# Optimization experiments

Hardware: AMD Instinct MI355X
Metric: run time of the kernel (lower is better)

The kernel has to match this reference:

```python
import jax, jax.numpy as jnp
import numpy as np

B, CIN, H, W = 32, 128, 64, 64
OUT, KH, KW = 256, 3, 3
NSK, SDIM = 4, 128


def setup_inputs() -> dict:
    key = jax.random.key(0)
    kx, kw_, kb, ks = jax.random.split(key, 4)
    x = jax.random.normal(kx, (B, CIN, H, W), dtype=jnp.float32)
    kval = float(np.sqrt(1.0 / (CIN * KH * KW)))  # groups=1
    weight = jax.random.uniform(kw_, (OUT, CIN, KH, KW), jnp.float32, -kval, kval)
    bias_tensor = jax.random.uniform(kb, (OUT,), jnp.float32, -kval, kval)
    # Rademacher / sketch_dim, shape (n, s, O) == torch's type1_signed_matrices
    signed = (2.0 * jax.random.bernoulli(ks, 0.5, (NSK, SDIM, OUT)).astype(jnp.float32) - 1.0) / SDIM
    # prod = einsum('ijkl,mi->mjkl') per sketch -> (n, s, Cin, kh, kw)
    prod = jnp.einsum('oikl,nso->nsikl', weight, signed)
    # .permute(2,3,1,0).flatten(0,2): (s,Cin,kh,kw) -> (kh,kw,Cin,s) -> (kh*kw*Cin, s)
    type1_sketches = prod.transpose(0, 3, 4, 2, 1).reshape(NSK, KH * KW * CIN, SDIM)
    return {
        "x": x,
        "type1_sketches": type1_sketches,
        "type1_signed_matrices": signed,
        "bias_tensor": bias_tensor,
    }


def reference(x, type1_sketches, type1_signed_matrices, bias_tensor):
    b, _, h1, w1 = x.shape
    h2 = h1 - KH + 1
    w2 = w1 - KW + 1
    # torch unfold: (B, Cin*KH*KW, E), features ordered channel-major (C, kh, kw)
    patches = jax.lax.conv_general_dilated_patches(
        x, filter_shape=(KH, KW), window_strides=(1, 1), padding='VALID'
    )  # (B, Cin*KH*KW, H2, W2)
    patches = patches.reshape(b, CIN * KH * KW, h2 * w2)  # (B, F, E)
    # 'bnfe,nfs->bnse' with the n-expansion folded away
    y = jnp.einsum('bfe,nfs->bnse', patches, type1_sketches)
    z = jnp.einsum('bnse,nso->bnoe', y, type1_signed_matrices)
    z = z.reshape(b, NSK, OUT, h2, w2)
    out = jnp.mean(z, axis=1) + bias_tensor[None, :, None, None]
    return out
```

## Files before the change

kernel.cpp:

```cpp
#include <hip/hip_runtime.h>
#include <hip/hip_bf16.h>
#include <stdint.h>


#define BATCH 32
#define CIN   128
#define HH    64
#define WW    64
#define OUTC  256
#define H2    62
#define W2    62
#define A_TILE 32768
#define WS_A_BYTES (18 * A_TILE)
#define BKHB  17408

typedef __bf16 bf16x8 __attribute__((ext_vector_type(8)));
typedef float  f32x4  __attribute__((ext_vector_type(4)));

typedef unsigned int u32_as1 __attribute__((address_space(1)));
typedef unsigned int u32_as3 __attribute__((address_space(3)));

__device__ __forceinline__ void async_copy16(const void* g, void* l) {
  __builtin_amdgcn_global_load_lds((const u32_as1*)g, (u32_as3*)l, 16, 0, 0);
}

#define FPB 4
__global__ __launch_bounds__(256) void weff_kernel(
    const float* __restrict__ sketches,
    const float* __restrict__ sgn,
    char* __restrict__ wsA)
{
  __shared__ alignas(16) float sk[512 * FPB];
  const int f0 = blockIdx.x * FPB;
  const int t  = threadIdx.x;

  for (int k = 0; k < (512 * FPB) / 256; ++k) {
    int idx = t + k * 256;
    int fi  = idx >> 9;
    int ns  = idx & 511;
    int n   = ns >> 7;
    int s   = ns & 127;
    sk[ns * FPB + fi] = sketches[(n * 1152 + f0 + fi) * 128 + s];
  }
  __syncthreads();

  const int o = t;
  float acc0 = 0.f, acc1 = 0.f, acc2 = 0.f, acc3 = 0.f;
#pragma unroll 8
  for (int ns = 0; ns < 512; ++ns) {
    float sg = sgn[ns * 256 + o];
    f32x4 skv = *(const f32x4*)(&sk[ns * FPB]);
    acc0 += sg * skv[0];
    acc1 += sg * skv[1];
    acc2 += sg * skv[2];
    acc3 += sg * skv[3];
  }

  float accs[FPB] = {acc0, acc1, acc2, acc3};
#pragma unroll
  for (int fi = 0; fi < FPB; ++fi) {
    int f    = f0 + fi;
    int c    = f / 9;
    int khkw = f - c * 9;
    int s    = khkw * 2 + (c >> 6);
    int kk   = c & 63;
    uint32_t byteoff = (uint32_t)s * A_TILE + (uint32_t)o * 128
                     + (((uint32_t)kk * 2u) ^ (uint32_t)((o & 7) << 4));
    *(__hip_bfloat16*)(wsA + byteoff) = __float2bfloat16(accs[fi] * 0.25f);
  }
}

__global__ __launch_bounds__(512, 2) void conv_kernel(
    const float* __restrict__ x,
    const char*  __restrict__ wA,
    const float* __restrict__ bias,
    float* __restrict__ out)
{
  __shared__ alignas(16) char lds[65536 + 4 * BKHB];
  char* ldsA = lds;
  char* ldsB = lds + 65536;

  const int bid = blockIdx.x;
  const int swz = (bid & 7) * 124 + (bid >> 3);
  const int b   = swz / 31;
  const int ip  = swz - b * 31;
  const int i0  = ip * 2;

  const int t    = threadIdx.x;
  const int lane = t & 63;
  const int w    = t >> 6;
  const int wo   = w >> 1;
  const int ir   = w & 1;

#define STAGE_A(LIN, BUF) do {                                             \
    const char* asrc_ = wA + (size_t)(LIN) * A_TILE + w * 1024 + lane * 16;\
    char* adst_ = ldsA + (BUF) * 32768 + w * 1024;                         \
    async_copy16(asrc_,          adst_);                                   \
    async_copy16(asrc_ + 8192,   adst_ + 8192);                            \
    async_copy16(asrc_ + 16384,  adst_ + 16384);                           \
    async_copy16(asrc_ + 24576,  adst_ + 24576);                           \
  } while (0)

  STAGE_A(0, 0);

  {
    const int j  = t & 63;
    const int cq = t >> 6;
    const uint32_t swb = (uint32_t)((j & 7) << 4);
#pragma unroll
    for (int r = 0; r < 4; ++r) {
      const float* xr = x + (((size_t)(b * CIN + cq * 16)) * HH + (i0 + r)) * WW + j;
      char* lrow = ldsB + r * BKHB + j * 256;
#pragma unroll
      for (int g = 0; g < 2; ++g) {
        bf16x8 pk;
#pragma unroll
        for (int cc = 0; cc < 8; ++cc)
          pk[cc] = (__bf16)xr[(size_t)(g * 8 + cc) * (HH * WW)];
        uint32_t c0b = (uint32_t)(cq * 32 + g * 16);
        *(bf16x8*)(lrow + (c0b ^ swb)) = pk;
      }
    }
    if (t < 256) {
      int r  = t >> 6;
      int pj = 64 + ((t >> 4) & 3);
      int sl = (t & 15) * 16;
      bf16x8 z = {};
      *(bf16x8*)(ldsB + r * BKHB + pj * 256 + sl) = z;
    }
  }

  f32x4 acc[4][4];
  const f32x4 zf = {0.f, 0.f, 0.f, 0.f};
#pragma unroll
  for (int mi = 0; mi < 4; ++mi)
#pragma unroll
    for (int ni = 0; ni < 4; ++ni)
      acc[mi][ni] = zf;

  __syncthreads();

  const int ln15  = lane & 15;
  const int khi16 = (lane >> 4) << 4;
  const uint32_t swa = (uint32_t)((ln15 & 7) << 4);
  const char* pAr = ldsA + (wo * 64 + ln15) * 128;
  const char* pA0 = pAr + (((uint32_t)khi16) ^ swa);
  const char* pA1 = pAr + (((uint32_t)(64 | khi16)) ^ swa);

#define MKB(KW, KS) (ldsB + ir * BKHB + (ln15 + (KW)) * 256                \
    + (((uint32_t)(((KS) << 6) | khi16)) ^ ((uint32_t)(((ln15 + (KW)) & 7) << 4))))
  const char* pB00 = MKB(0, 0); const char* pB01 = MKB(0, 1);
  const char* pB10 = MKB(1, 0); const char* pB11 = MKB(1, 1);
  const char* pB20 = MKB(2, 0); const char* pB21 = MKB(2, 1);
#undef MKB

#define MFMA_ __builtin_amdgcn_mfma_f32_16x16x32_bf16

#define KSBLK(LIN, KH, KW, KS) do {                                        \
    const int ai_ = ((LIN) & 1) * 32768;                                   \
    bf16x8 a0_ = *(const bf16x8*)(pA##KS + ai_);                           \
    bf16x8 a1_ = *(const bf16x8*)(pA##KS + ai_ + 2048);                    \
    bf16x8 a2_ = *(const bf16x8*)(pA##KS + ai_ + 4096);                    \
    bf16x8 a3_ = *(const bf16x8*)(pA##KS + ai_ + 6144);                    \
    const int bi_ = (KH) * BKHB + ((LIN) & 1) * 128;                       \
    bf16x8 b0_ = *(const bf16x8*)(pB##KW##KS + bi_);                       \
    bf16x8 b1_ = *(const bf16x8*)(pB##KW##KS + bi_ + 4096);                \
    bf16x8 b2_ = *(const bf16x8*)(pB##KW##KS + bi_ + 8192);                \
    bf16x8 b3_ = *(const bf16x8*)(pB##KW##KS + bi_ + 12288);               \
    acc[0][0] = MFMA_(a0_, b0_, acc[0][0], 0, 0, 0);                       \
    acc[0][1] = MFMA_(a0_, b1_, acc[0][1], 0, 0, 0);                       \
    acc[0][2] = MFMA_(a0_, b2_, acc[0][2], 0, 0, 0);                       \
    acc[0][3] = MFMA_(a0_, b3_, acc[0][3], 0, 0, 0);                       \
    acc[1][0] = MFMA_(a1_, b0_, acc[1][0], 0, 0, 0);                       \
    acc[1][1] = MFMA_(a1_, b1_, acc[1][1], 0, 0, 0);                       \
    acc[1][2] = MFMA_(a1_, b2_, acc[1][2], 0, 0, 0);                       \
    acc[1][3] = MFMA_(a1_, b3_, acc[1][3], 0, 0, 0);                       \
    acc[2][0] = MFMA_(a2_, b0_, acc[2][0], 0, 0, 0);                       \
    acc[2][1] = MFMA_(a2_, b1_, acc[2][1], 0, 0, 0);                       \
    acc[2][2] = MFMA_(a2_, b2_, acc[2][2], 0, 0, 0);                       \
    acc[2][3] = MFMA_(a2_, b3_, acc[2][3], 0, 0, 0);                       \
    acc[3][0] = MFMA_(a3_, b0_, acc[3][0], 0, 0, 0);                       \
    acc[3][1] = MFMA_(a3_, b1_, acc[3][1], 0, 0, 0);                       \
    acc[3][2] = MFMA_(a3_, b2_, acc[3][2], 0, 0, 0);                       \
    acc[3][3] = MFMA_(a3_, b3_, acc[3][3], 0, 0, 0);                       \
  } while (0)

#define STEP(LIN, KH, KW) do {                                             \
    if ((LIN) < 17) STAGE_A((LIN) + 1, ((LIN) + 1) & 1);                   \
    KSBLK(LIN, KH, KW, 0);                                                 \
    KSBLK(LIN, KH, KW, 1);                                                 \
    __syncthreads();                                                       \
  } while (0)

  STEP(0, 0, 0);   STEP(1, 0, 0);
  STEP(2, 0, 1);   STEP(3, 0, 1);
  STEP(4, 0, 2);   STEP(5, 0, 2);
  STEP(6, 1, 0);   STEP(7, 1, 0);
  STEP(8, 1, 1);   STEP(9, 1, 1);
  STEP(10, 1, 2);  STEP(11, 1, 2);
  STEP(12, 2, 0);  STEP(13, 2, 0);
  STEP(14, 2, 1);  STEP(15, 2, 1);
  STEP(16, 2, 2);  STEP(17, 2, 2);

#undef STEP
#undef KSBLK
#undef MFMA_
#undef STAGE_A

  const int jn   = ln15;
  const int g4   = lane >> 4;
  const int irow = i0 + ir;
#pragma unroll
  for (int mi = 0; mi < 4; ++mi) {
#pragma unroll
    for (int ni = 0; ni < 4; ++ni) {
      const int jj = (ni << 4) + jn;
      if (jj < W2) {
#pragma unroll
        for (int rr = 0; rr < 4; ++rr) {
          const int o = (wo << 6) + (mi << 4) + (g4 << 2) + rr;
          out[(((size_t)b * OUTC + o) * H2 + irow) * W2 + jj] = acc[mi][ni][rr] + bias[o];
        }
      }
    }
  }
}

extern "C" void kernel_launch(void* const* d_in, const int* in_sizes, int n_in,
                              void* d_out, int out_size, void* d_ws, size_t ws_size,
                              hipStream_t stream) {
  const float* x        = (const float*)d_in[0];
  const float* sketches = (const float*)d_in[1];
  const float* sgn      = (const float*)d_in[2];
  const float* bias     = (const float*)d_in[3];
  float* out            = (float*)d_out;
  char* wsA             = (char*)d_ws;

  if (ws_size < (size_t)WS_A_BYTES) return;

  weff_kernel<<<1152 / FPB, 256, 0, stream>>>(sketches, sgn, wsA);
  conv_kernel<<<BATCH * (H2 / 2), 512, 0, stream>>>(x, wsA, bias, out);
}
```

Before: 115.4 us.

## Prefetch two A stages ahead with explicit waitcnt and split barriers

Moves the weight-tile async copies two stages ahead and replaces the per-step __syncthreads with explicit vmcnt/lgkmcnt waits and raw s_barrier. All LDS fragments for a step are loaded into registers first, then the buffer is released and the next copy issued so it overlaps the MFMA block, which runs at raised priority. The aim is to hide global-to-LDS latency and cut barrier stalls. It relies on hand-counted vmcnt values matching the outstanding async copies, and it raises register pressure from holding 16 fragments at once.

```diff
diff --git a/kernel.cpp b/kernel.cpp
--- a/kernel.cpp
+++ b/kernel.cpp
@@ -102,6 +102,7 @@
   } while (0)
 
   STAGE_A(0, 0);
+  STAGE_A(1, 1);
 
   {
     const int j  = t & 63;
@@ -138,8 +139,6 @@
     for (int ni = 0; ni < 4; ++ni)
       acc[mi][ni] = zf;
 
-  __syncthreads();
-
   const int ln15  = lane & 15;
   const int khi16 = (lane >> 4) << 4;
   const uint32_t swa = (uint32_t)((ln15 & 7) << 4);
@@ -154,56 +153,88 @@
   const char* pB20 = MKB(2, 0); const char* pB21 = MKB(2, 1);
 #undef MKB
 
+  asm volatile("s_waitcnt lgkmcnt(0)" ::: "memory");
+
 #define MFMA_ __builtin_amdgcn_mfma_f32_16x16x32_bf16
-
-#define KSBLK(LIN, KH, KW, KS) do {                                        \
-    const int ai_ = ((LIN) & 1) * 32768;                                   \
-    bf16x8 a0_ = *(const bf16x8*)(pA##KS + ai_);                           \
-    bf16x8 a1_ = *(const bf16x8*)(pA##KS + ai_ + 2048);                    \
-    bf16x8 a2_ = *(const bf16x8*)(pA##KS + ai_ + 4096);                    \
-    bf16x8 a3_ = *(const bf16x8*)(pA##KS + ai_ + 6144);                    \
-    const int bi_ = (KH) * BKHB + ((LIN) & 1) * 128;                       \
-    bf16x8 b0_ = *(const bf16x8*)(pB##KW##KS + bi_);                       \
-    bf16x8 b1_ = *(const bf16x8*)(pB##KW##KS + bi_ + 4096);                \
-    bf16x8 b2_ = *(const bf16x8*)(pB##KW##KS + bi_ + 8192);                \
-    bf16x8 b3_ = *(const bf16x8*)(pB##KW##KS + bi_ + 12288);               \
-    acc[0][0] = MFMA_(a0_, b0_, acc[0][0], 0, 0, 0);                       \
-    acc[0][1] = MFMA_(a0_, b1_, acc[0][1], 0, 0, 0);                       \
-    acc[0][2] = MFMA_(a0_, b2_, acc[0][2], 0, 0, 0);                       \
-    acc[0][3] = MFMA_(a0_, b3_, acc[0][3], 0, 0, 0);                       \
-    acc[1][0] = MFMA_(a1_, b0_, acc[1][0], 0, 0, 0);                       \
-    acc[1][1] = MFMA_(a1_, b1_, acc[1][1], 0, 0, 0);                       \
-    acc[1][2] = MFMA_(a1_, b2_, acc[1][2], 0, 0, 0);                       \
-    acc[1][3] = MFMA_(a1_, b3_, acc[1][3], 0, 0, 0);                       \
-    acc[2][0] = MFMA_(a2_, b0_, acc[2][0], 0, 0, 0);                       \
-    acc[2][1] = MFMA_(a2_, b1_, acc[2][1], 0, 0, 0);                       \
-    acc[2][2] = MFMA_(a2_, b2_, acc[2][2], 0, 0, 0);                       \
-    acc[2][3] = MFMA_(a2_, b3_, acc[2][3], 0, 0, 0);                       \
-    acc[3][0] = MFMA_(a3_, b0_, acc[3][0], 0, 0, 0);                       \
-    acc[3][1] = MFMA_(a3_, b1_, acc[3][1], 0, 0, 0);                       \
-    acc[3][2] = MFMA_(a3_, b2_, acc[3][2], 0, 0, 0);                       \
-    acc[3][3] = MFMA_(a3_, b3_, acc[3][3], 0, 0, 0);                       \
+#define WAITVM4 asm volatile("s_waitcnt vmcnt(4)" ::: "memory")
+#define WAITVM0 asm volatile("s_waitcnt vmcnt(0)" ::: "memory")
+#define WAITLG0 asm volatile("s_waitcnt lgkmcnt(0)" ::: "memory")
+
+#define STEP(LIN, KH, KW, WVM) do {                                        \
+    WVM;                                                                   \
+    __builtin_amdgcn_s_barrier();                                          \
+    const int ai_  = ((LIN) & 1) * 32768;                                  \
+    const int chb_ = ((LIN) & 1) * 128 + (KH) * BKHB;                      \
+    bf16x8 aA0 = *(const bf16x8*)(pA0 + ai_);                              \
+    bf16x8 aA1 = *(const bf16x8*)(pA0 + ai_ + 2048);                       \
+    bf16x8 aA2 = *(const bf16x8*)(pA0 + ai_ + 4096);                       \
+    bf16x8 aA3 = *(const bf16x8*)(pA0 + ai_ + 6144);                       \
+    bf16x8 aB0 = *(const bf16x8*)(pA1 + ai_);                              \
+    bf16x8 aB1 = *(const bf16x8*)(pA1 + ai_ + 2048);                       \
+    bf16x8 aB2 = *(const bf16x8*)(pA1 + ai_ + 4096);                       \
+    bf16x8 aB3 = *(const bf16x8*)(pA1 + ai_ + 6144);                       \
+    bf16x8 bA0 = *(const bf16x8*)(pB##KW##0 + chb_);                       \
+    bf16x8 bA1 = *(const bf16x8*)(pB##KW##0 + chb_ + 4096);                \
+    bf16x8 bA2 = *(const bf16x8*)(pB##KW##0 + chb_ + 8192);                \
+    bf16x8 bA3 = *(const bf16x8*)(pB##KW##0 + chb_ + 12288);               \
+    bf16x8 bB0 = *(const bf16x8*)(pB##KW##1 + chb_);                       \
+    bf16x8 bB1 = *(const bf16x8*)(pB##KW##1 + chb_ + 4096);                \
+    bf16x8 bB2 = *(const bf16x8*)(pB##KW##1 + chb_ + 8192);                \
+    bf16x8 bB3 = *(const bf16x8*)(pB##KW##1 + chb_ + 12288);               \
+    WAITLG0;                                                               \
+    __builtin_amdgcn_sched_barrier(0);                                     \
+    __builtin_amdgcn_s_barrier();                                          \
+    if ((LIN) < 16) STAGE_A((LIN) + 2, (LIN) & 1);                         \
+    __builtin_amdgcn_s_setprio(1);                                         \
+    acc[0][0] = MFMA_(aA0, bA0, acc[0][0], 0, 0, 0);                       \
+    acc[0][1] = MFMA_(aA0, bA1, acc[0][1], 0, 0, 0);                       \
+    acc[0][2] = MFMA_(aA0, bA2, acc[0][2], 0, 0, 0);                       \
+    acc[0][3] = MFMA_(aA0, bA3, acc[0][3], 0, 0, 0);                       \
+    acc[1][0] = MFMA_(aA1, bA0, acc[1][0], 0, 0, 0);                       \
+    acc[1][1] = MFMA_(aA1, bA1, acc[1][1], 0, 0, 0);                       \
+    acc[1][2] = MFMA_(aA1, bA2, acc[1][2], 0, 0, 0);                       \
+    acc[1][3] = MFMA_(aA1, bA3, acc[1][3], 0, 0, 0);                       \
+    acc[2][0] = MFMA_(aA2, bA0, acc[2][0], 0, 0, 0);                       \
+    acc[2][1] = MFMA_(aA2, bA1, acc[2][1], 0, 0, 0);                       \
+    acc[2][2] = MFMA_(aA2, bA2, acc[2][2], 0, 0, 0);                       \
+    acc[2][3] = MFMA_(aA2, bA3, acc[2][3], 0, 0, 0);                       \
+    acc[3][0] = MFMA_(aA3, bA0, acc[3][0], 0, 0, 0);                       \
+    acc[3][1] = MFMA_(aA3, bA1, acc[3][1], 0, 0, 0);                       \
+    acc[3][2] = MFMA_(aA3, bA2, acc[3][2], 0, 0, 0);                       \
+    acc[3][3] = MFMA_(aA3, bA3, acc[3][3], 0, 0, 0);                       \
+    acc[0][0] = MFMA_(aB0, bB0, acc[0][0], 0, 0, 0);                       \
+    acc[0][1] = MFMA_(aB0, bB1, acc[0][1], 0, 0, 0);                       \
+    acc[0][2] = MFMA_(aB0, bB2, acc[0][2], 0, 0, 0);                       \
+    acc[0][3] = MFMA_(aB0, bB3, acc[0][3], 0, 0, 0);                       \
+    acc[1][0] = MFMA_(aB1, bB0, acc[1][0], 0, 0, 0);                       \
+    acc[1][1] = MFMA_(aB1, bB1, acc[1][1], 0, 0, 0);                       \
+    acc[1][2] = MFMA_(aB1, bB2, acc[1][2], 0, 0, 0);                       \
+    acc[1][3] = MFMA_(aB1, bB3, acc[1][3], 0, 0, 0);                       \
+    acc[2][0] = MFMA_(aB2, bB0, acc[2][0], 0, 0, 0);                       \
+    acc[2][1] = MFMA_(aB2, bB1, acc[2][1], 0, 0, 0);                       \
+    acc[2][2] = MFMA_(aB2, bB2, acc[2][2], 0, 0, 0);                       \
+    acc[2][3] = MFMA_(aB2, bB3, acc[2][3], 0, 0, 0);                       \
+    acc[3][0] = MFMA_(aB3, bB0, acc[3][0], 0, 0, 0);                       \
+    acc[3][1] = MFMA_(aB3, bB1, acc[3][1], 0, 0, 0);                       \
+    acc[3][2] = MFMA_(aB3, bB2, acc[3][2], 0, 0, 0);                       \
+    acc[3][3] = MFMA_(aB3, bB3, acc[3][3], 0, 0, 0);                       \
+    __builtin_amdgcn_s_setprio(0);                                         \
   } while (0)
 
-#define STEP(LIN, KH, KW) do {                                             \
-    if ((LIN) < 17) STAGE_A((LIN) + 1, ((LIN) + 1) & 1);                   \
-    KSBLK(LIN, KH, KW, 0);                                                 \
-    KSBLK(LIN, KH, KW, 1);                                                 \
-    __syncthreads();                                                       \
-  } while (0)
-
-  STEP(0, 0, 0);   STEP(1, 0, 0);
-  STEP(2, 0, 1);   STEP(3, 0, 1);
-  STEP(4, 0, 2);   STEP(5, 0, 2);
-  STEP(6, 1, 0);   STEP(7, 1, 0);
-  STEP(8, 1, 1);   STEP(9, 1, 1);
-  STEP(10, 1, 2);  STEP(11, 1, 2);
-  STEP(12, 2, 0);  STEP(13, 2, 0);
-  STEP(14, 2, 1);  STEP(15, 2, 1);
-  STEP(16, 2, 2);  STEP(17, 2, 2);
+  STEP(0, 0, 0, WAITVM4);   STEP(1, 0, 0, WAITVM4);
+  STEP(2, 0, 1, WAITVM4);   STEP(3, 0, 1, WAITVM4);
+  STEP(4, 0, 2, WAITVM4);   STEP(5, 0, 2, WAITVM4);
+  STEP(6, 1, 0, WAITVM4);   STEP(7, 1, 0, WAITVM4);
+  STEP(8, 1, 1, WAITVM4);   STEP(9, 1, 1, WAITVM4);
+  STEP(10, 1, 2, WAITVM4);  STEP(11, 1, 2, WAITVM4);
+  STEP(12, 2, 0, WAITVM4);  STEP(13, 2, 0, WAITVM4);
+  STEP(14, 2, 1, WAITVM4);  STEP(15, 2, 1, WAITVM4);
+  STEP(16, 2, 2, WAITVM4);  STEP(17, 2, 2, WAITVM0);
 
 #undef STEP
-#undef KSBLK
+#undef WAITLG0
+#undef WAITVM0
+#undef WAITVM4
 #undef MFMA_
 #undef STAGE_A
 
```

Result: slower. 129.0 us (+11.8%).

## Enlarge conv tile to four output rows with 128-channel warp tiles

Applied to the files above, without the earlier changes.

Each block now computes four output rows (16 row groups per image, 512 blocks) instead of two. Each warp covers 128 output channels by one row, using an 8x4 accumulator tile, so every B fragment is reused across twice as many A fragments. This halves the number of times each weight tile is staged per output and removes the final barrier. The row halo is clamped and the last-column fragment uses clamped pointers instead of zero padding. In exchange the kernel needs more registers and LDS (6 input rows), and the last row group computes rows that are discarded.

```diff
diff --git a/kernel.cpp b/kernel.cpp
--- a/kernel.cpp
+++ b/kernel.cpp
@@ -12,7 +12,7 @@
 #define W2    62
 #define A_TILE 32768
 #define WS_A_BYTES (18 * A_TILE)
-#define BKHB  17408
+#define BROWB 16384
 
 typedef __bf16 bf16x8 __attribute__((ext_vector_type(8)));
 typedef float  f32x4  __attribute__((ext_vector_type(4)));
@@ -76,21 +76,21 @@
     const float* __restrict__ bias,
     float* __restrict__ out)
 {
-  __shared__ alignas(16) char lds[65536 + 4 * BKHB];
+  __shared__ alignas(16) char lds[65536 + 6 * BROWB];
   char* ldsA = lds;
   char* ldsB = lds + 65536;
 
   const int bid = blockIdx.x;
-  const int swz = (bid & 7) * 124 + (bid >> 3);
-  const int b   = swz / 31;
-  const int ip  = swz - b * 31;
-  const int i0  = ip * 2;
+  const int swz = (bid & 7) * 64 + (bid >> 3);
+  const int b   = swz >> 4;
+  const int ig  = swz & 15;
+  const int i0  = ig * 4;
 
   const int t    = threadIdx.x;
   const int lane = t & 63;
   const int w    = t >> 6;
-  const int wo   = w >> 1;
-  const int ir   = w & 1;
+  const int wo   = w >> 2;
+  const int we   = w & 3;
 
 #define STAGE_A(LIN, BUF) do {                                             \
     const char* asrc_ = wA + (size_t)(LIN) * A_TILE + w * 1024 + lane * 16;\
@@ -108,9 +108,10 @@
     const int cq = t >> 6;
     const uint32_t swb = (uint32_t)((j & 7) << 4);
 #pragma unroll
-    for (int r = 0; r < 4; ++r) {
-      const float* xr = x + (((size_t)(b * CIN + cq * 16)) * HH + (i0 + r)) * WW + j;
-      char* lrow = ldsB + r * BKHB + j * 256;
+    for (int r = 0; r < 6; ++r) {
+      int xrow = i0 + r; if (xrow > 63) xrow = 63;
+      const float* xr = x + (((size_t)(b * CIN + cq * 16)) * HH + xrow) * WW + j;
+      char* lrow = ldsB + r * BROWB + j * 256;
 #pragma unroll
       for (int g = 0; g < 2; ++g) {
         bf16x8 pk;
@@ -121,52 +122,53 @@
         *(bf16x8*)(lrow + (c0b ^ swb)) = pk;
       }
     }
-    if (t < 256) {
-      int r  = t >> 6;
-      int pj = 64 + ((t >> 4) & 3);
-      int sl = (t & 15) * 16;
-      bf16x8 z = {};
-      *(bf16x8*)(ldsB + r * BKHB + pj * 256 + sl) = z;
-    }
-  }
-
-  f32x4 acc[4][4];
+  }
+
+  f32x4 acc[8][4];
   const f32x4 zf = {0.f, 0.f, 0.f, 0.f};
 #pragma unroll
-  for (int mi = 0; mi < 4; ++mi)
+  for (int mi = 0; mi < 8; ++mi)
 #pragma unroll
     for (int ni = 0; ni < 4; ++ni)
       acc[mi][ni] = zf;
-
-  __syncthreads();
 
   const int ln15  = lane & 15;
   const int khi16 = (lane >> 4) << 4;
   const uint32_t swa = (uint32_t)((ln15 & 7) << 4);
-  const char* pAr = ldsA + (wo * 64 + ln15) * 128;
+  const char* pAr = ldsA + (wo * 128 + ln15) * 128;
   const char* pA0 = pAr + (((uint32_t)khi16) ^ swa);
   const char* pA1 = pAr + (((uint32_t)(64 | khi16)) ^ swa);
 
-#define MKB(KW, KS) (ldsB + ir * BKHB + (ln15 + (KW)) * 256                \
-    + (((uint32_t)(((KS) << 6) | khi16)) ^ ((uint32_t)(((ln15 + (KW)) & 7) << 4))))
-  const char* pB00 = MKB(0, 0); const char* pB01 = MKB(0, 1);
-  const char* pB10 = MKB(1, 0); const char* pB11 = MKB(1, 1);
-  const char* pB20 = MKB(2, 0); const char* pB21 = MKB(2, 1);
+#define MKB(COL, KS) (ldsB + (we * 64 + (COL)) * 256                       \
+    + (((uint32_t)(((KS) << 6) | khi16)) ^ ((uint32_t)(((COL) & 7) << 4))))
+  const char* pB00 = MKB(ln15 + 0, 0); const char* pB01 = MKB(ln15 + 0, 1);
+  const char* pB10 = MKB(ln15 + 1, 0); const char* pB11 = MKB(ln15 + 1, 1);
+  const char* pB20 = MKB(ln15 + 2, 0); const char* pB21 = MKB(ln15 + 2, 1);
+  const int c30 = (48 + ln15 + 0 > 63) ? 63 : 48 + ln15 + 0;
+  const int c31 = (48 + ln15 + 1 > 63) ? 63 : 48 + ln15 + 1;
+  const int c32 = (48 + ln15 + 2 > 63) ? 63 : 48 + ln15 + 2;
+  const char* pC00 = MKB(c30, 0); const char* pC01 = MKB(c30, 1);
+  const char* pC10 = MKB(c31, 0); const char* pC11 = MKB(c31, 1);
+  const char* pC20 = MKB(c32, 0); const char* pC21 = MKB(c32, 1);
 #undef MKB
 
+  __syncthreads();
+
 #define MFMA_ __builtin_amdgcn_mfma_f32_16x16x32_bf16
 
-#define KSBLK(LIN, KH, KW, KS) do {                                        \
-    const int ai_ = ((LIN) & 1) * 32768;                                   \
-    bf16x8 a0_ = *(const bf16x8*)(pA##KS + ai_);                           \
-    bf16x8 a1_ = *(const bf16x8*)(pA##KS + ai_ + 2048);                    \
-    bf16x8 a2_ = *(const bf16x8*)(pA##KS + ai_ + 4096);                    \
-    bf16x8 a3_ = *(const bf16x8*)(pA##KS + ai_ + 6144);                    \
-    const int bi_ = (KH) * BKHB + ((LIN) & 1) * 128;                       \
-    bf16x8 b0_ = *(const bf16x8*)(pB##KW##KS + bi_);                       \
-    bf16x8 b1_ = *(const bf16x8*)(pB##KW##KS + bi_ + 4096);                \
-    bf16x8 b2_ = *(const bf16x8*)(pB##KW##KS + bi_ + 8192);                \
-    bf16x8 b3_ = *(const bf16x8*)(pB##KW##KS + bi_ + 12288);               \
+#define KSH(AP, BP, CP, IMM, AIMM) do {                                    \
+    bf16x8 b0_ = *(const bf16x8*)((BP) + (IMM));                           \
+    bf16x8 b1_ = *(const bf16x8*)((BP) + (IMM) + 4096);                    \
+    bf16x8 b2_ = *(const bf16x8*)((BP) + (IMM) + 8192);                    \
+    bf16x8 b3_ = *(const bf16x8*)((CP) + (IMM));                           \
+    bf16x8 a0_ = *(const bf16x8*)((AP) + (AIMM));                          \
+    bf16x8 a1_ = *(const bf16x8*)((AP) + (AIMM) + 2048);                   \
+    bf16x8 a2_ = *(const bf16x8*)((AP) + (AIMM) + 4096);                   \
+    bf16x8 a3_ = *(const bf16x8*)((AP) + (AIMM) + 6144);                   \
+    bf16x8 a4_ = *(const bf16x8*)((AP) + (AIMM) + 8192);                   \
+    bf16x8 a5_ = *(const bf16x8*)((AP) + (AIMM) + 10240);                  \
+    bf16x8 a6_ = *(const bf16x8*)((AP) + (AIMM) + 12288);                  \
+    bf16x8 a7_ = *(const bf16x8*)((AP) + (AIMM) + 14336);                  \
     acc[0][0] = MFMA_(a0_, b0_, acc[0][0], 0, 0, 0);                       \
     acc[0][1] = MFMA_(a0_, b1_, acc[0][1], 0, 0, 0);                       \
     acc[0][2] = MFMA_(a0_, b2_, acc[0][2], 0, 0, 0);                       \
@@ -183,13 +185,31 @@
     acc[3][1] = MFMA_(a3_, b1_, acc[3][1], 0, 0, 0);                       \
     acc[3][2] = MFMA_(a3_, b2_, acc[3][2], 0, 0, 0);                       \
     acc[3][3] = MFMA_(a3_, b3_, acc[3][3], 0, 0, 0);                       \
+    acc[4][0] = MFMA_(a4_, b0_, acc[4][0], 0, 0, 0);                       \
+    acc[4][1] = MFMA_(a4_, b1_, acc[4][1], 0, 0, 0);                       \
+    acc[4][2] = MFMA_(a4_, b2_, acc[4][2], 0, 0, 0);                       \
+    acc[4][3] = MFMA_(a4_, b3_, acc[4][3], 0, 0, 0);                       \
+    acc[5][0] = MFMA_(a5_, b0_, acc[5][0], 0, 0, 0);                       \
+    acc[5][1] = MFMA_(a5_, b1_, acc[5][1], 0, 0, 0);                       \
+    acc[5][2] = MFMA_(a5_, b2_, acc[5][2], 0, 0, 0);                       \
+    acc[5][3] = MFMA_(a5_, b3_, acc[5][3], 0, 0, 0);                       \
+    acc[6][0] = MFMA_(a6_, b0_, acc[6][0], 0, 0, 0);                       \
+    acc[6][1] = MFMA_(a6_, b1_, acc[6][1], 0, 0, 0);                       \
+    acc[6][2] = MFMA_(a6_, b2_, acc[6][2], 0, 0, 0);                       \
+    acc[6][3] = MFMA_(a6_, b3_, acc[6][3], 0, 0, 0);                       \
+    acc[7][0] = MFMA_(a7_, b0_, acc[7][0], 0, 0, 0);                       \
+    acc[7][1] = MFMA_(a7_, b1_, acc[7][1], 0, 0, 0);                       \
+    acc[7][2] = MFMA_(a7_, b2_, acc[7][2], 0, 0, 0);                       \
+    acc[7][3] = MFMA_(a7_, b3_, acc[7][3], 0, 0, 0);                       \
   } while (0)
 
 #define STEP(LIN, KH, KW) do {                                             \
     if ((LIN) < 17) STAGE_A((LIN) + 1, ((LIN) + 1) & 1);                   \
-    KSBLK(LIN, KH, KW, 0);                                                 \
-    KSBLK(LIN, KH, KW, 1);                                                 \
-    __syncthreads();                                                       \
+    KSH(pA0, pB##KW##0, pC##KW##0,                                         \
+        (KH) * BROWB + ((LIN) & 1) * 128, ((LIN) & 1) * 32768);            \
+    KSH(pA1, pB##KW##1, pC##KW##1,                                         \
+        (KH) * BROWB + ((LIN) & 1) * 128, ((LIN) & 1) * 32768);            \
+    if ((LIN) < 17) __syncthreads();                                       \
   } while (0)
 
   STEP(0, 0, 0);   STEP(1, 0, 0);
@@ -203,23 +223,26 @@
   STEP(16, 2, 2);  STEP(17, 2, 2);
 
 #undef STEP
-#undef KSBLK
+#undef KSH
 #undef MFMA_
 #undef STAGE_A
 
   const int jn   = ln15;
   const int g4   = lane >> 4;
-  const int irow = i0 + ir;
-#pragma unroll
-  for (int mi = 0; mi < 4; ++mi) {
-#pragma unroll
-    for (int ni = 0; ni < 4; ++ni) {
-      const int jj = (ni << 4) + jn;
-      if (jj < W2) {
-#pragma unroll
-        for (int rr = 0; rr < 4; ++rr) {
-          const int o = (wo << 6) + (mi << 4) + (g4 << 2) + rr;
-          out[(((size_t)b * OUTC + o) * H2 + irow) * W2 + jj] = acc[mi][ni][rr] + bias[o];
+  const int irow = i0 + we;
+  if (irow < H2) {
+#pragma unroll
+    for (int mi = 0; mi < 8; ++mi) {
+#pragma unroll
+      for (int ni = 0; ni < 4; ++ni) {
+        const int jj = (ni << 4) + jn;
+        if (jj < W2) {
+#pragma unroll
+          for (int rr = 0; rr < 4; ++rr) {
+            const int o = (wo << 7) + (mi << 4) + (g4 << 2) + rr;
+            out[(((size_t)b * OUTC + o) * H2 + irow) * W2 + jj] =
+                acc[mi][ni][rr] + bias[o];
+          }
         }
       }
     }
@@ -239,5 +262,5 @@
   if (ws_size < (size_t)WS_A_BYTES) return;
 
   weff_kernel<<<1152 / FPB, 256, 0, stream>>>(sketches, sgn, wsA);
-  conv_kernel<<<BATCH * (H2 / 2), 512, 0, stream>>>(x, wsA, bias, out);
-}
+  conv_kernel<<<BATCH * 16, 512, 0, stream>>>(x, wsA, bias, out);
+}
```

Result: faster. 106.5 us (-7.7%).

## Retile conv kernel to one output row per block with finer weight stages

Applied to the files above, without the earlier changes.

The conv kernel now has each 256-thread block compute a single output row instead of two, with 4 waves each owning 64 output channels. The weight matrix is re-laid out in the workspace into 36 smaller stages (32 channels per stage) in a fragment-friendly order, so A operand loads are contiguous per lane without XOR swizzle. The last N-tile clamps column indices instead of zero-padding LDS, and MFMA bursts are wrapped in s_setprio. Input rows are no longer shared between two output rows, so each block stages three input rows for one output row, and the extra stages add more barriers.

```diff
diff --git a/kernel.cpp b/kernel.cpp
--- a/kernel.cpp
+++ b/kernel.cpp
@@ -10,9 +10,9 @@
 #define OUTC  256
 #define H2    62
 #define W2    62
-#define A_TILE 32768
-#define WS_A_BYTES (18 * A_TILE)
-#define BKHB  17408
+#define A_TILE 16384
+#define WS_A_BYTES (36 * A_TILE)
+#define BROWB 16384
 
 typedef __bf16 bf16x8 __attribute__((ext_vector_type(8)));
 typedef float  f32x4  __attribute__((ext_vector_type(4)));
@@ -59,46 +59,44 @@
   float accs[FPB] = {acc0, acc1, acc2, acc3};
 #pragma unroll
   for (int fi = 0; fi < FPB; ++fi) {
-    int f    = f0 + fi;
-    int c    = f / 9;
-    int khkw = f - c * 9;
-    int s    = khkw * 2 + (c >> 6);
-    int kk   = c & 63;
-    uint32_t byteoff = (uint32_t)s * A_TILE + (uint32_t)o * 128
-                     + (((uint32_t)kk * 2u) ^ (uint32_t)((o & 7) << 4));
+    int f   = f0 + fi;
+    int c   = f / 9;
+    int tap = f - c * 9;
+    int st  = tap * 4 + (c >> 5);
+    int kk  = c & 31;
+    uint32_t byteoff = (uint32_t)st * A_TILE + (uint32_t)(o >> 4) * 1024
+                     + (uint32_t)(((kk >> 3) * 16 + (o & 15)) * 16)
+                     + (uint32_t)((kk & 7) * 2);
     *(__hip_bfloat16*)(wsA + byteoff) = __float2bfloat16(accs[fi] * 0.25f);
   }
 }
 
-__global__ __launch_bounds__(512, 2) void conv_kernel(
+__global__ __launch_bounds__(256, 2) void conv_kernel(
     const float* __restrict__ x,
     const char*  __restrict__ wA,
     const float* __restrict__ bias,
     float* __restrict__ out)
 {
-  __shared__ alignas(16) char lds[65536 + 4 * BKHB];
+  __shared__ alignas(16) char lds[2 * A_TILE + 3 * BROWB];
   char* ldsA = lds;
-  char* ldsB = lds + 65536;
+  char* ldsB = lds + 2 * A_TILE;
 
   const int bid = blockIdx.x;
-  const int swz = (bid & 7) * 124 + (bid >> 3);
-  const int b   = swz / 31;
-  const int ip  = swz - b * 31;
-  const int i0  = ip * 2;
+  const int swz = (bid & 7) * 248 + (bid >> 3);
+  const int b   = swz / H2;
+  const int i   = swz - b * H2;
 
   const int t    = threadIdx.x;
   const int lane = t & 63;
   const int w    = t >> 6;
-  const int wo   = w >> 1;
-  const int ir   = w & 1;
-
-#define STAGE_A(LIN, BUF) do {                                             \
-    const char* asrc_ = wA + (size_t)(LIN) * A_TILE + w * 1024 + lane * 16;\
-    char* adst_ = ldsA + (BUF) * 32768 + w * 1024;                         \
-    async_copy16(asrc_,          adst_);                                   \
-    async_copy16(asrc_ + 8192,   adst_ + 8192);                            \
-    async_copy16(asrc_ + 16384,  adst_ + 16384);                           \
-    async_copy16(asrc_ + 24576,  adst_ + 24576);                           \
+
+#define STAGE_A(ST, BUF) do {                                              \
+    const char* asrc_ = wA + (size_t)(ST) * A_TILE + w * 4096 + lane * 16; \
+    char* adst_ = ldsA + (BUF) * A_TILE + w * 4096;                        \
+    async_copy16(asrc_,         adst_);                                    \
+    async_copy16(asrc_ + 1024,  adst_ + 1024);                             \
+    async_copy16(asrc_ + 2048,  adst_ + 2048);                             \
+    async_copy16(asrc_ + 3072,  adst_ + 3072);                             \
   } while (0)
 
   STAGE_A(0, 0);
@@ -108,26 +106,19 @@
     const int cq = t >> 6;
     const uint32_t swb = (uint32_t)((j & 7) << 4);
 #pragma unroll
-    for (int r = 0; r < 4; ++r) {
-      const float* xr = x + (((size_t)(b * CIN + cq * 16)) * HH + (i0 + r)) * WW + j;
-      char* lrow = ldsB + r * BKHB + j * 256;
-#pragma unroll
-      for (int g = 0; g < 2; ++g) {
+    for (int r = 0; r < 3; ++r) {
+      const float* xr = x + (((size_t)(b * CIN + cq * 32)) * HH + (i + r)) * WW + j;
+      char* lrow = ldsB + r * BROWB + j * 256;
+#pragma unroll
+      for (int g = 0; g < 4; ++g) {
         bf16x8 pk;
 #pragma unroll
         for (int cc = 0; cc < 8; ++cc)
           pk[cc] = (__bf16)xr[(size_t)(g * 8 + cc) * (HH * WW)];
-        uint32_t c0b = (uint32_t)(cq * 32 + g * 16);
+        uint32_t c0b = (uint32_t)(cq * 64 + g * 16);
         *(bf16x8*)(lrow + (c0b ^ swb)) = pk;
       }
     }
-    if (t < 256) {
-      int r  = t >> 6;
-      int pj = 64 + ((t >> 4) & 3);
-      int sl = (t & 15) * 16;
-      bf16x8 z = {};
-      *(bf16x8*)(ldsB + r * BKHB + pj * 256 + sl) = z;
-    }
   }
 
   f32x4 acc[4][4];
@@ -138,35 +129,40 @@
     for (int ni = 0; ni < 4; ++ni)
       acc[mi][ni] = zf;
 
-  __syncthreads();
-
   const int ln15  = lane & 15;
   const int khi16 = (lane >> 4) << 4;
-  const uint32_t swa = (uint32_t)((ln15 & 7) << 4);
-  const char* pAr = ldsA + (wo * 64 + ln15) * 128;
-  const char* pA0 = pAr + (((uint32_t)khi16) ^ swa);
-  const char* pA1 = pAr + (((uint32_t)(64 | khi16)) ^ swa);
-
-#define MKB(KW, KS) (ldsB + ir * BKHB + (ln15 + (KW)) * 256                \
-    + (((uint32_t)(((KS) << 6) | khi16)) ^ ((uint32_t)(((ln15 + (KW)) & 7) << 4))))
-  const char* pB00 = MKB(0, 0); const char* pB01 = MKB(0, 1);
-  const char* pB10 = MKB(1, 0); const char* pB11 = MKB(1, 1);
-  const char* pB20 = MKB(2, 0); const char* pB21 = MKB(2, 1);
+  const char* pA = ldsA + w * 4096 + lane * 16;
+
+#define MKB(COL, PAR) (ldsB + (COL) * 256                                  \
+    + (uint32_t)((((PAR) * 64) | khi16) ^ (((COL) & 7) << 4)))
+  const char* pB00 = MKB(ln15 + 0, 0); const char* pB01 = MKB(ln15 + 0, 1);
+  const char* pB10 = MKB(ln15 + 1, 0); const char* pB11 = MKB(ln15 + 1, 1);
+  const char* pB20 = MKB(ln15 + 2, 0); const char* pB21 = MKB(ln15 + 2, 1);
+  const int c30 = (48 + ln15 + 0 > 63) ? 63 : 48 + ln15 + 0;
+  const int c31 = (48 + ln15 + 1 > 63) ? 63 : 48 + ln15 + 1;
+  const int c32 = (48 + ln15 + 2 > 63) ? 63 : 48 + ln15 + 2;
+  const char* pC00 = MKB(c30, 0); const char* pC01 = MKB(c30, 1);
+  const char* pC10 = MKB(c31, 0); const char* pC11 = MKB(c31, 1);
+  const char* pC20 = MKB(c32, 0); const char* pC21 = MKB(c32, 1);
 #undef MKB
 
+  __syncthreads();
+
 #define MFMA_ __builtin_amdgcn_mfma_f32_16x16x32_bf16
 
-#define KSBLK(LIN, KH, KW, KS) do {                                        \
-    const int ai_ = ((LIN) & 1) * 32768;                                   \
-    bf16x8 a0_ = *(const bf16x8*)(pA##KS + ai_);                           \
-    bf16x8 a1_ = *(const bf16x8*)(pA##KS + ai_ + 2048);                    \
-    bf16x8 a2_ = *(const bf16x8*)(pA##KS + ai_ + 4096);                    \
-    bf16x8 a3_ = *(const bf16x8*)(pA##KS + ai_ + 6144);                    \
-    const int bi_ = (KH) * BKHB + ((LIN) & 1) * 128;                       \
-    bf16x8 b0_ = *(const bf16x8*)(pB##KW##KS + bi_);                       \
-    bf16x8 b1_ = *(const bf16x8*)(pB##KW##KS + bi_ + 4096);                \
-    bf16x8 b2_ = *(const bf16x8*)(pB##KW##KS + bi_ + 8192);                \
-    bf16x8 b3_ = *(const bf16x8*)(pB##KW##KS + bi_ + 12288);               \
+#define STEP(ST, KH, KW, CK2, PAR) do {                                    \
+    if ((ST) < 35) STAGE_A((ST) + 1, ((ST) + 1) & 1);                      \
+    const int ab_ = ((ST) & 1) * A_TILE;                                   \
+    const int bi_ = (KH) * BROWB + (CK2) * 128;                            \
+    bf16x8 b0_ = *(const bf16x8*)(pB##KW##PAR + bi_);                      \
+    bf16x8 b1_ = *(const bf16x8*)(pB##KW##PAR + bi_ + 4096);               \
+    bf16x8 b2_ = *(const bf16x8*)(pB##KW##PAR + bi_ + 8192);               \
+    bf16x8 b3_ = *(const bf16x8*)(pC##KW##PAR + bi_);                      \
+    bf16x8 a0_ = *(const bf16x8*)(pA + ab_);                               \
+    bf16x8 a1_ = *(const bf16x8*)(pA + ab_ + 1024);                        \
+    bf16x8 a2_ = *(const bf16x8*)(pA + ab_ + 2048);                        \
+    bf16x8 a3_ = *(const bf16x8*)(pA + ab_ + 3072);                        \
+    __builtin_amdgcn_s_setprio(1);                                         \
     acc[0][0] = MFMA_(a0_, b0_, acc[0][0], 0, 0, 0);                       \
     acc[0][1] = MFMA_(a0_, b1_, acc[0][1], 0, 0, 0);                       \
     acc[0][2] = MFMA_(a0_, b2_, acc[0][2], 0, 0, 0);                       \
@@ -183,33 +179,35 @@
     acc[3][1] = MFMA_(a3_, b1_, acc[3][1], 0, 0, 0);                       \
     acc[3][2] = MFMA_(a3_, b2_, acc[3][2], 0, 0, 0);                       \
     acc[3][3] = MFMA_(a3_, b3_, acc[3][3], 0, 0, 0);                       \
+    __builtin_amdgcn_s_setprio(0);                                         \
+    if ((ST) < 35) __syncthreads();                                        \
   } while (0)
 
-#define STEP(LIN, KH, KW) do {                                             \
-    if ((LIN) < 17) STAGE_A((LIN) + 1, ((LIN) + 1) & 1);                   \
-    KSBLK(LIN, KH, KW, 0);                                                 \
-    KSBLK(LIN, KH, KW, 1);                                                 \
-    __syncthreads();                                                       \
-  } while (0)
-
-  STEP(0, 0, 0);   STEP(1, 0, 0);
-  STEP(2, 0, 1);   STEP(3, 0, 1);
-  STEP(4, 0, 2);   STEP(5, 0, 2);
-  STEP(6, 1, 0);   STEP(7, 1, 0);
-  STEP(8, 1, 1);   STEP(9, 1, 1);
-  STEP(10, 1, 2);  STEP(11, 1, 2);
-  STEP(12, 2, 0);  STEP(13, 2, 0);
-  STEP(14, 2, 1);  STEP(15, 2, 1);
-  STEP(16, 2, 2);  STEP(17, 2, 2);
+  STEP(0,  0, 0, 0, 0);  STEP(1,  0, 0, 0, 1);
+  STEP(2,  0, 0, 1, 0);  STEP(3,  0, 0, 1, 1);
+  STEP(4,  0, 1, 0, 0);  STEP(5,  0, 1, 0, 1);
+  STEP(6,  0, 1, 1, 0);  STEP(7,  0, 1, 1, 1);
+  STEP(8,  0, 2, 0, 0);  STEP(9,  0, 2, 0, 1);
+  STEP(10, 0, 2, 1, 0);  STEP(11, 0, 2, 1, 1);
+  STEP(12, 1, 0, 0, 0);  STEP(13, 1, 0, 0, 1);
+  STEP(14, 1, 0, 1, 0);  STEP(15, 1, 0, 1, 1);
+  STEP(16, 1, 1, 0, 0);  STEP(17, 1, 1, 0, 1);
+  STEP(18, 1, 1, 1, 0);  STEP(19, 1, 1, 1, 1);
+  STEP(20, 1, 2, 0, 0);  STEP(21, 1, 2, 0, 1);
+  STEP(22, 1, 2, 1, 0);  STEP(23, 1, 2, 1, 1);
+  STEP(24, 2, 0, 0, 0);  STEP(25, 2, 0, 0, 1);
+  STEP(26, 2, 0, 1, 0);  STEP(27, 2, 0, 1, 1);
+  STEP(28, 2, 1, 0, 0);  STEP(29, 2, 1, 0, 1);
+  STEP(30, 2, 1, 1, 0);  STEP(31, 2, 1, 1, 1);
+  STEP(32, 2, 2, 0, 0);  STEP(33, 2, 2, 0, 1);
+  STEP(34, 2, 2, 1, 0);  STEP(35, 2, 2, 1, 1);
 
 #undef STEP
-#undef KSBLK
 #undef MFMA_
 #undef STAGE_A
 
-  const int jn   = ln15;
-  const int g4   = lane >> 4;
-  const int irow = i0 + ir;
+  const int jn = ln15;
+  const int g4 = lane >> 4;
 #pragma unroll
   for (int mi = 0; mi < 4; ++mi) {
 #pragma unroll
@@ -218,8 +216,9 @@
       if (jj < W2) {
 #pragma unroll
         for (int rr = 0; rr < 4; ++rr) {
-          const int o = (wo << 6) + (mi << 4) + (g4 << 2) + rr;
-          out[(((size_t)b * OUTC + o) * H2 + irow) * W2 + jj] = acc[mi][ni][rr] + bias[o];
+          const int o = (w << 6) + (mi << 4) + (g4 << 2) + rr;
+          out[(((size_t)b * OUTC + o) * H2 + i) * W2 + jj] =
+              acc[mi][ni][rr] + bias[o];
         }
       }
     }
@@ -239,5 +238,5 @@
   if (ws_size < (size_t)WS_A_BYTES) return;
 
   weff_kernel<<<1152 / FPB, 256, 0, stream>>>(sketches, sgn, wsA);
-  conv_kernel<<<BATCH * (H2 / 2), 512, 0, stream>>>(x, wsA, bias, out);
-}
+  conv_kernel<<<BATCH * H2, 256, 0, stream>>>(x, wsA, bias, out);
+}
```

After: 124.7 us. 8.1% more time.
